# Optimization experiments

Measured on AMD Instinct MI355X. Metric: run time of the kernel, lower is better.

## Reference

```python
import jax, jax.numpy as jnp
import numpy as np

B, N, D = 8, 8192, 512
HID_ATT = D // 8          # input_dim // num_heads = 64
TOPK = max(1, int(N * 0.3))  # 2457


def _mlp2(x, W1, b1, W2, b2):
    # 2-layer MLP: Linear -> GELU -> Linear (inference mode: dropout/norm off)
    h = jax.nn.gelu(x @ W1 + b1)
    return h @ W2 + b2


def setup_inputs() -> dict:
    key = jax.random.key(0)
    ks = jax.random.split(key, 9)
    s = lambda k, sh, fan: jax.random.normal(k, sh, jnp.float32) * (1.0 / np.sqrt(fan))
    return {
        "x": jax.random.normal(ks[0], (B, N, D), jnp.float32),
        # attention-score MLP: D -> HID_ATT -> 1
        "aW1": s(ks[1], (D, HID_ATT), D),
        "ab1": jnp.zeros((HID_ATT,), jnp.float32),
        "aW2": s(ks[2], (HID_ATT, 1), HID_ATT),
        "ab2": jnp.zeros((1,), jnp.float32),
        # projection MLP: D -> D -> D
        "pW1": s(ks[3], (D, D), D),
        "pb1": jnp.zeros((D,), jnp.float32),
        "pW2": s(ks[4], (D, D), D),
        "pb2": jnp.zeros((D,), jnp.float32),
    }


def reference(x, aW1, ab1, aW2, ab2, pW1, pb1, pW2, pb2):
    # per-instance attention score -> sigmoid weight, [B, N]
    weights = jax.nn.sigmoid(_mlp2(x, aW1, ab1, aW2, ab2)[..., 0])
    # top-k per bag (largest)
    topk_scores, topk_idx = jax.lax.top_k(weights, TOPK)  # [B, TOPK]
    # gather selected instances, scale by score, mean over selected -> [B, D]
    sel = jnp.take_along_axis(x, topk_idx[..., None], axis=1)  # [B, TOPK, D]
    emb = jnp.mean(sel * topk_scores[..., None], axis=1)       # [B, D]
    projection = _mlp2(emb, pW1, pb1, pW2, pb2)                # [B, D]
    return projection, weights
```

## Files before the change

### kernel.cpp

```cpp
#include <hip/hip_runtime.h>
#include <math.h>

#define B_BAGS 8
#define N_INST 8192
#define D_DIM  512
#define H_ATT  64
#define TOPK_K 2457
#define ROWS_TOTAL (B_BAGS * N_INST)

typedef __attribute__((ext_vector_type(8))) short bf16x8;
typedef __attribute__((ext_vector_type(4))) float f32x4;

#define WS_W1P_HI 0
#define WS_W1P_LO 65536
#define WS_PART3  131584
#define WS_PART1  (WS_PART3 + 8*64*512*4)
#define WS_THRESH (WS_PART1 + 16*8*512*4)

__device__ __forceinline__ unsigned short bf16_rn(float f) {
  unsigned int x = __float_as_uint(f);
  unsigned int r = (x + 0x7FFFu + ((x >> 16) & 1u)) >> 16;
  return (unsigned short)r;
}
__device__ __forceinline__ float bf16_f(unsigned short u) {
  return __uint_as_float(((unsigned int)u) << 16);
}
__device__ __forceinline__ float gelu_f(float v) {
  float u = 0.7978845608028654f * (v + 0.044715f * v * v * v);
  return 0.5f * v * (1.0f + tanhf(u));
}

__device__ __forceinline__ void cvt_hilo(const float4 u, const float4 v,
                                         bf16x8& h, bf16x8& l) {
  float f[8] = {u.x, u.y, u.z, u.w, v.x, v.y, v.z, v.w};
#pragma unroll
  for (int i = 0; i < 8; i++) {
    unsigned int b = __float_as_uint(f[i]);
    unsigned int hb = b & 0xFFFF0000u;
    float r = f[i] - __uint_as_float(hb);
    h[i] = (short)(b >> 16);
    l[i] = (short)(__float_as_uint(r) >> 16);
  }
}

__device__ __forceinline__ void load_lds16(const void* g, void* l) {
  __builtin_amdgcn_global_load_lds(
      (const __attribute__((address_space(1))) void*)g,
      (__attribute__((address_space(3))) void*)l, 16, 0, 0);
}

__global__ __launch_bounds__(256) void k_prep(const float* __restrict__ aW1,
                                              unsigned short* __restrict__ hi,
                                              unsigned short* __restrict__ lo) {
  int tau = blockIdx.x * 256 + threadIdx.x;
  if (tau >= 4096) return;
  int ks = tau >> 8, t = (tau >> 6) & 3, lane = tau & 63;
  int n = t * 16 + (lane & 15);
  int kb = ks * 32 + (lane >> 4) * 8;
#pragma unroll
  for (int j = 0; j < 8; j++) {
    float v = aW1[(kb + j) * H_ATT + n];
    unsigned short h = bf16_rn(v);
    unsigned short l = bf16_rn(v - bf16_f(h));
    hi[tau * 8 + j] = h;
    lo[tau * 8 + j] = l;
  }
}

#define BM 64
#define AUNIT 1040

__global__ __launch_bounds__(256) void k_scores(
    const float* __restrict__ x,
    const unsigned short* __restrict__ w1p_hi,
    const unsigned short* __restrict__ w1p_lo,
    const float* __restrict__ ab1, const float* __restrict__ aW2,
    const float* __restrict__ ab2, float* __restrict__ wout) {
  __shared__ __align__(16) char Asm[16 * AUNIT];
  __shared__ __align__(16) char Bh[8192];
  __shared__ __align__(16) char Bl[8192];

  int tid = threadIdx.x;
  int wave = tid >> 6, lane = tid & 63;
  int c0 = lane & 15, quad = lane >> 4;
  int rowBase0 = blockIdx.x * BM;

  f32x4 acc[4];
#pragma unroll
  for (int t = 0; t < 4; t++) acc[t] = (f32x4){0.f, 0.f, 0.f, 0.f};

  const int r = wave * 16 + c0;
  const int uA = r >> 2;
  const int aoff = uA * AUNIT + (r & 3) * 256 + quad * 32;

  for (int c = 0; c < 8; c++) {
    size_t kb = (size_t)c * 256;
#pragma unroll
    for (int i = 0; i < 4; i++) {
      int u = wave * 4 + i;
      const char* g = (const char*)x +
          (size_t)(rowBase0 + u * 4 + (lane >> 4)) * 2048 + kb + (size_t)(lane & 15) * 16;
      load_lds16(g, Asm + u * AUNIT);
    }
#pragma unroll
    for (int i = 0; i < 4; i++) {
      int v = wave * 4 + i;
      int vv = v & 7;
      const char* gsrc = (v < 8) ? (const char*)w1p_hi : (const char*)w1p_lo;
      char* ldst = (v < 8) ? Bh : Bl;
      load_lds16(gsrc + (size_t)c * 8192 + vv * 1024 + (size_t)lane * 16,
                 ldst + vv * 1024);
    }
    __syncthreads();

#pragma unroll
    for (int stp = 0; stp < 2; stp++) {
      const float4 a0v = *reinterpret_cast<const float4*>(Asm + aoff + stp * 128);
      const float4 a1v = *reinterpret_cast<const float4*>(Asm + aoff + stp * 128 + 16);
      bf16x8 afh, afl;
      cvt_hilo(a0v, a1v, afh, afl);
      bf16x8 bfh[4], bfl[4];
#pragma unroll
      for (int t = 0; t < 4; t++) {
        bfh[t] = *reinterpret_cast<const bf16x8*>(Bh + (stp * 4 + t) * 1024 + lane * 16);
        bfl[t] = *reinterpret_cast<const bf16x8*>(Bl + (stp * 4 + t) * 1024 + lane * 16);
      }
#pragma unroll
      for (int t = 0; t < 4; t++) {
        acc[t] = __builtin_amdgcn_mfma_f32_16x16x32_bf16(afl, bfh[t], acc[t], 0, 0, 0);
        acc[t] = __builtin_amdgcn_mfma_f32_16x16x32_bf16(afh, bfl[t], acc[t], 0, 0, 0);
        acc[t] = __builtin_amdgcn_mfma_f32_16x16x32_bf16(afh, bfh[t], acc[t], 0, 0, 0);
      }
    }
    __syncthreads();
  }

  float w2v[4], b1v[4];
#pragma unroll
  for (int t = 0; t < 4; t++) {
    w2v[t] = aW2[t * 16 + c0];
    b1v[t] = ab1[t * 16 + c0];
  }
  float bias2 = ab2[0];
  float p[4] = {0.f, 0.f, 0.f, 0.f};
#pragma unroll
  for (int t = 0; t < 4; t++)
#pragma unroll
    for (int rr = 0; rr < 4; rr++) {
      float h = gelu_f(acc[t][rr] + b1v[t]);
      p[rr] += h * w2v[t];
    }
#pragma unroll
  for (int off = 1; off < 16; off <<= 1)
#pragma unroll
    for (int rr = 0; rr < 4; rr++) p[rr] += __shfl_xor(p[rr], off, 64);
  if (c0 == 0) {
    int row = rowBase0 + wave * 16 + quad * 4;
#pragma unroll
    for (int rr = 0; rr < 4; rr++) {
      float sc = p[rr] + bias2;
      wout[row + rr] = 1.0f / (1.0f + expf(-sc));
    }
  }
}

__global__ __launch_bounds__(256) void k_thresh(const float* __restrict__ wout,
                                                unsigned int* __restrict__ thr) {
  int b = blockIdx.x;
  int tid = threadIdx.x;
  const float* w = wout + b * N_INST;

  unsigned int v[32];
#pragma unroll
  for (int j = 0; j < 32; j++) v[j] = __float_as_uint(w[j * 256 + tid]);

  __shared__ int red[2][4];
  int lane = tid & 63, wv = tid >> 6;
  int pb = 0;
  auto blocksum = [&](int c) -> int {
#pragma unroll
    for (int off = 32; off > 0; off >>= 1) c += __shfl_down(c, off, 64);
    if (lane == 0) red[pb][wv] = c;
    __syncthreads();
    int s = red[pb][0] + red[pb][1] + red[pb][2] + red[pb][3];
    pb ^= 1;
    return s;
  };

  unsigned int lo = 0u, hi = 0x3F800001u;
  while (hi - lo > 1u) {
    unsigned int mid = lo + ((hi - lo) >> 1);
    int c = 0;
#pragma unroll
    for (int j = 0; j < 32; j++) c += (v[j] >= mid) ? 1 : 0;
    if (blocksum(c) >= TOPK_K) lo = mid; else hi = mid;
  }
  unsigned int T = lo;
  int c1 = 0;
#pragma unroll
  for (int j = 0; j < 32; j++) c1 += (v[j] > T) ? 1 : 0;
  c1 = blocksum(c1);
  int needed = TOPK_K - c1;
  unsigned int tm = 0;
#pragma unroll
  for (int j = 0; j < 32; j++) tm |= (v[j] == T ? 1u : 0u) << j;
  int lom = -1, him = N_INST - 1;
  while (him - lom > 1) {
    int mid = (lom + him) >> 1;
    unsigned int mask = 0u;
    if (mid >= tid) {
      unsigned int jmax = (unsigned int)(mid - tid) >> 8;
      mask = (2u << jmax) - 1u;
    }
    if (blocksum((int)__popc(tm & mask)) >= needed) him = mid; else lom = mid;
  }
  if (tid == 0) {
    thr[b * 2] = T;
    thr[b * 2 + 1] = (unsigned int)him;
  }
}

__global__ __launch_bounds__(256) void k_gather(const float* __restrict__ x,
                                                const float* __restrict__ wout,
                                                const unsigned int* __restrict__ thr,
                                                float* __restrict__ part3) {
  int b = blockIdx.x >> 6;
  int blk = blockIdx.x & 63;
  int tid = threadIdx.x;
  const float* w = wout + b * N_INST;

  unsigned int T = thr[b * 2];
  int Icut = (int)thr[b * 2 + 1];

  __shared__ int idxs[128];
  __shared__ float wgts[128];
  __shared__ int wcnt[2];
  __shared__ float4 xfer[128];

  int lane = tid & 63;
  int r = blk * 128 + tid;
  bool sel = false;
  float wvv = 0.f;
  int pos = 0;
  if (tid < 128) {
    wvv = w[r];
    unsigned int wu = __float_as_uint(wvv);
    sel = (wu > T) || (wu == T && r <= Icut);
    unsigned long long m = __ballot(sel);
    pos = __popcll(m & ((1ull << lane) - 1ull));
    if (lane == 0) wcnt[tid >> 6] = __popcll(m);
  }
  __syncthreads();
  int total = wcnt[0] + wcnt[1];
  if (sel) {
    int base = (tid >= 64) ? wcnt[0] : 0;
    idxs[base + pos] = r;
    wgts[base + pos] = wvv;
  }
  __syncthreads();

  int half = tid >> 7;
  int L = tid & 127;
  float4 acc = {0.f, 0.f, 0.f, 0.f};
  const float* xb = x + (size_t)b * N_INST * D_DIM;
  int i2 = total & ~1;
#pragma unroll 4
  for (int i = 0; i < i2; i += 2) {
    int rr = idxs[i + half];
    float ww = wgts[i + half];
    const float4 xv = *reinterpret_cast<const float4*>(xb + (size_t)rr * D_DIM + L * 4);
    acc.x += ww * xv.x; acc.y += ww * xv.y; acc.z += ww * xv.z; acc.w += ww * xv.w;
  }
  if ((total & 1) && half == 0) {
    int rr = idxs[i2];
    float ww = wgts[i2];
    const float4 xv = *reinterpret_cast<const float4*>(xb + (size_t)rr * D_DIM + L * 4);
    acc.x += ww * xv.x; acc.y += ww * xv.y; acc.z += ww * xv.z; acc.w += ww * xv.w;
  }
  if (half == 1) xfer[L] = acc;
  __syncthreads();
  if (half == 0) {
    float4 o = xfer[L];
    acc.x += o.x; acc.y += o.y; acc.z += o.z; acc.w += o.w;
    *reinterpret_cast<float4*>(part3 + (size_t)(b * 64 + blk) * D_DIM + L * 4) = acc;
  }
}

__global__ __launch_bounds__(256) void k_proj1(const float* __restrict__ part3,
                                               const float* __restrict__ pW1,
                                               float* __restrict__ part1,
                                               const float* __restrict__ pb2,
                                               float* __restrict__ out) {
  int jt = blockIdx.x & 7, kt = blockIdx.x >> 3;
  __shared__ float emb_s[256];
  int tid = threadIdx.x;
  int col = tid & 63, bg = tid >> 6;
  if (kt == 0) {
    float bz = pb2[jt * 64 + col];
    out[(bg * 2) * 512 + jt * 64 + col] = bz;
    out[(bg * 2 + 1) * 512 + jt * 64 + col] = bz;
  }
  {
    int b = tid >> 5, d0 = tid & 31;
    const float* p = part3 + (size_t)b * 64 * 512 + kt * 32 + d0;
    float e = 0.f;
#pragma unroll 8
    for (int j = 0; j < 64; j++) e += p[j * 512];
    emb_s[b * 32 + d0] = e * (1.0f / TOPK_K);
  }
  __syncthreads();
  float a0 = 0.f, a1 = 0.f;
  const float* wrow = pW1 + (size_t)(kt * 32) * 512 + jt * 64 + col;
#pragma unroll 8
  for (int q = 0; q < 32; q++) {
    float wq = wrow[q * 512];
    a0 += emb_s[(bg * 2) * 32 + q] * wq;
    a1 += emb_s[(bg * 2 + 1) * 32 + q] * wq;
  }
  part1[kt * 4096 + (bg * 2) * 512 + jt * 64 + col] = a0;
  part1[kt * 4096 + (bg * 2 + 1) * 512 + jt * 64 + col] = a1;
}

__global__ __launch_bounds__(256) void k_proj2(const float* __restrict__ part1,
                                               const float* __restrict__ pb1,
                                               const float* __restrict__ pW2,
                                               float* __restrict__ out) {
  int jt = blockIdx.x & 7, kt = blockIdx.x >> 3;
  __shared__ float h_s[256];
  int tid = threadIdx.x;
  {
    int b = tid >> 5, j0 = tid & 31;
    int jj = kt * 32 + j0;
    float s = pb1[jj];
#pragma unroll
    for (int p = 0; p < 16; p++) s += part1[p * 4096 + b * 512 + jj];
    h_s[b * 32 + j0] = gelu_f(s);
  }
  __syncthreads();
  int col = tid & 63, bg = tid >> 6;
  float a0 = 0.f, a1 = 0.f;
  const float* wrow = pW2 + (size_t)(kt * 32) * 512 + jt * 64 + col;
#pragma unroll 8
  for (int q = 0; q < 32; q++) {
    float wq = wrow[q * 512];
    a0 += h_s[(bg * 2) * 32 + q] * wq;
    a1 += h_s[(bg * 2 + 1) * 32 + q] * wq;
  }
  atomicAdd(&out[(bg * 2) * 512 + jt * 64 + col], a0);
  atomicAdd(&out[(bg * 2 + 1) * 512 + jt * 64 + col], a1);
}

extern "C" void kernel_launch(void* const* d_in, const int* in_sizes, int n_in,
                              void* d_out, int out_size, void* d_ws, size_t ws_size,
                              hipStream_t stream) {
  (void)in_sizes; (void)n_in; (void)out_size; (void)ws_size;
  const float* x   = (const float*)d_in[0];
  const float* aW1 = (const float*)d_in[1];
  const float* ab1 = (const float*)d_in[2];
  const float* aW2 = (const float*)d_in[3];
  const float* ab2 = (const float*)d_in[4];
  const float* pW1 = (const float*)d_in[5];
  const float* pb1 = (const float*)d_in[6];
  const float* pW2 = (const float*)d_in[7];
  const float* pb2 = (const float*)d_in[8];

  float* out  = (float*)d_out;
  float* wout = out + B_BAGS * D_DIM;

  char* ws = (char*)d_ws;
  unsigned short* w1p_hi = (unsigned short*)(ws + WS_W1P_HI);
  unsigned short* w1p_lo = (unsigned short*)(ws + WS_W1P_LO);
  float* part3 = (float*)(ws + WS_PART3);
  float* part1 = (float*)(ws + WS_PART1);
  unsigned int* thr = (unsigned int*)(ws + WS_THRESH);

  k_prep<<<dim3(16), dim3(256), 0, stream>>>(aW1, w1p_hi, w1p_lo);
  k_scores<<<dim3(ROWS_TOTAL / BM), dim3(256), 0, stream>>>(x, w1p_hi, w1p_lo, ab1, aW2, ab2, wout);
  k_thresh<<<dim3(B_BAGS), dim3(256), 0, stream>>>(wout, thr);
  k_gather<<<dim3(B_BAGS * 64), dim3(256), 0, stream>>>(x, wout, thr, part3);
  k_proj1<<<dim3(128), dim3(256), 0, stream>>>(part3, pW1, part1, pb2, out);
  k_proj2<<<dim3(128), dim3(256), 0, stream>>>(part1, pb1, pW2, out);
}
```

Measured before the change: 254.7 us.

## Double-buffer LDS staging in score kernel to overlap loads with MFMA

The attention-score GEMM kernel now splits the K dimension into 16 smaller chunks and double-buffers the x tile and packed W1 hi/lo tiles in LDS. The next chunk is issued before computing on the current one, and there is one barrier per iteration instead of two. This is meant to hide global-to-LDS latency behind the MFMA work. The cost is more loop iterations with less work each, and correctness depends on the async LDS loads completing before the barrier.

```diff
diff --git a/kernel.cpp b/kernel.cpp
--- a/kernel.cpp
+++ b/kernel.cpp
@@ -68,7 +68,9 @@
 }
 
 #define BM 64
-#define AUNIT 1040
+#define NCH 16
+#define AUNIT2 1040
+#define ABUF (8 * AUNIT2)
 
 __global__ __launch_bounds__(256) void k_scores(
     const float* __restrict__ x,
@@ -76,9 +78,9 @@
     const unsigned short* __restrict__ w1p_lo,
     const float* __restrict__ ab1, const float* __restrict__ aW2,
     const float* __restrict__ ab2, float* __restrict__ wout) {
-  __shared__ __align__(16) char Asm[16 * AUNIT];
-  __shared__ __align__(16) char Bh[8192];
-  __shared__ __align__(16) char Bl[8192];
+  __shared__ __align__(16) char Asm[2][ABUF];
+  __shared__ __align__(16) char Bhs[2][4096];
+  __shared__ __align__(16) char Bls[2][4096];
 
   int tid = threadIdx.x;
   int wave = tid >> 6, lane = tid & 63;
@@ -90,47 +92,45 @@
   for (int t = 0; t < 4; t++) acc[t] = (f32x4){0.f, 0.f, 0.f, 0.f};
 
   const int r = wave * 16 + c0;
-  const int uA = r >> 2;
-  const int aoff = uA * AUNIT + (r & 3) * 256 + quad * 32;
-
-  for (int c = 0; c < 8; c++) {
-    size_t kb = (size_t)c * 256;
-#pragma unroll
-    for (int i = 0; i < 4; i++) {
-      int u = wave * 4 + i;
+  const int aoff = (r >> 3) * AUNIT2 + (r & 7) * 128 + quad * 32;
+
+  auto stage = [&](int c, int pb) {
+#pragma unroll
+    for (int i = 0; i < 2; i++) {
+      int u = wave * 2 + i;
       const char* g = (const char*)x +
-          (size_t)(rowBase0 + u * 4 + (lane >> 4)) * 2048 + kb + (size_t)(lane & 15) * 16;
-      load_lds16(g, Asm + u * AUNIT);
-    }
-#pragma unroll
-    for (int i = 0; i < 4; i++) {
-      int v = wave * 4 + i;
-      int vv = v & 7;
-      const char* gsrc = (v < 8) ? (const char*)w1p_hi : (const char*)w1p_lo;
-      char* ldst = (v < 8) ? Bh : Bl;
-      load_lds16(gsrc + (size_t)c * 8192 + vv * 1024 + (size_t)lane * 16,
-                 ldst + vv * 1024);
-    }
-    __syncthreads();
-
-#pragma unroll
-    for (int stp = 0; stp < 2; stp++) {
-      const float4 a0v = *reinterpret_cast<const float4*>(Asm + aoff + stp * 128);
-      const float4 a1v = *reinterpret_cast<const float4*>(Asm + aoff + stp * 128 + 16);
-      bf16x8 afh, afl;
-      cvt_hilo(a0v, a1v, afh, afl);
-      bf16x8 bfh[4], bfl[4];
-#pragma unroll
-      for (int t = 0; t < 4; t++) {
-        bfh[t] = *reinterpret_cast<const bf16x8*>(Bh + (stp * 4 + t) * 1024 + lane * 16);
-        bfl[t] = *reinterpret_cast<const bf16x8*>(Bl + (stp * 4 + t) * 1024 + lane * 16);
-      }
-#pragma unroll
-      for (int t = 0; t < 4; t++) {
-        acc[t] = __builtin_amdgcn_mfma_f32_16x16x32_bf16(afl, bfh[t], acc[t], 0, 0, 0);
-        acc[t] = __builtin_amdgcn_mfma_f32_16x16x32_bf16(afh, bfl[t], acc[t], 0, 0, 0);
-        acc[t] = __builtin_amdgcn_mfma_f32_16x16x32_bf16(afh, bfh[t], acc[t], 0, 0, 0);
-      }
+          (size_t)(rowBase0 + u * 8 + (lane >> 3)) * 2048 +
+          (size_t)c * 128 + (size_t)(lane & 7) * 16;
+      load_lds16(g, &Asm[pb][u * AUNIT2]);
+    }
+    load_lds16((const char*)w1p_hi + (size_t)c * 4096 + wave * 1024 + lane * 16,
+               &Bhs[pb][wave * 1024]);
+    load_lds16((const char*)w1p_lo + (size_t)c * 4096 + wave * 1024 + lane * 16,
+               &Bls[pb][wave * 1024]);
+  };
+
+  stage(0, 0);
+  __syncthreads();
+
+  for (int c = 0; c < NCH; c++) {
+    int pb = c & 1;
+    if (c + 1 < NCH) stage(c + 1, pb ^ 1);
+
+    const float4 a0v = *reinterpret_cast<const float4*>(&Asm[pb][aoff]);
+    const float4 a1v = *reinterpret_cast<const float4*>(&Asm[pb][aoff + 16]);
+    bf16x8 afh, afl;
+    cvt_hilo(a0v, a1v, afh, afl);
+    bf16x8 bfh[4], bfl[4];
+#pragma unroll
+    for (int t = 0; t < 4; t++) {
+      bfh[t] = *reinterpret_cast<const bf16x8*>(&Bhs[pb][t * 1024 + lane * 16]);
+      bfl[t] = *reinterpret_cast<const bf16x8*>(&Bls[pb][t * 1024 + lane * 16]);
+    }
+#pragma unroll
+    for (int t = 0; t < 4; t++) {
+      acc[t] = __builtin_amdgcn_mfma_f32_16x16x32_bf16(afl, bfh[t], acc[t], 0, 0, 0);
+      acc[t] = __builtin_amdgcn_mfma_f32_16x16x32_bf16(afh, bfl[t], acc[t], 0, 0, 0);
+      acc[t] = __builtin_amdgcn_mfma_f32_16x16x32_bf16(afh, bfh[t], acc[t], 0, 0, 0);
     }
     __syncthreads();
   }
```

Result: no change. 256.4 us (+0.7%).
